# Performance work log

Measured on AMD Instinct MI355X. Metric: run time of the kernel, lower is better.

Reference implementation:

```python
import jax, jax.numpy as jnp
import numpy as np
from jax import lax

L_TAU = 0.8
NUM_TIME = 20
B, H, W = 128, 64, 64
FLAT = 6 * 27 * 27  # 4374 features after conv(k=10)->55x55 and maxpool2 -> 27x27

def setup_inputs() -> dict:
    key = jax.random.key(0)
    k1, k2, k3, k4, k5, k6 = jax.random.split(key, 6)
    x = jax.random.uniform(k1, (B, H * W, NUM_TIME), dtype=jnp.float32)
    y = jax.random.randint(k2, (B,), 0, 2, dtype=jnp.int64)
    Wc = jax.random.normal(k3, (6, 1, 10, 10), dtype=jnp.float32) * 0.1  # OIHW
    bc = jnp.zeros((6,), dtype=jnp.float32)
    W2 = jax.random.normal(k4, (FLAT, 2), dtype=jnp.float32) * (1.0 / np.sqrt(FLAT))
    b2 = jnp.zeros((2,), dtype=jnp.float32)
    return {"x": x, "y": y, "Wc": Wc, "bc": bc, "W2": W2, "b2": b2}

def _maxpool2(a):
    return lax.reduce_window(a, -jnp.inf, lax.max,
                             (1, 1, 2, 2), (1, 1, 2, 2), 'VALID')

def _snu_forward(x, Wc, bc, W2, b2):
    xt = jnp.transpose(x, (2, 0, 1)).reshape(NUM_TIME, B, 1, H, W)  # [T,B,1,64,64]
    s1 = jnp.zeros((B, 6, 55, 55), jnp.float32); y1 = jnp.zeros_like(s1)
    s2 = jnp.zeros((B, 2), jnp.float32);        y2 = jnp.zeros_like(s2)

    def step(carry, x_t):
        s1, y1, s2, y2 = carry
        c = lax.conv_general_dilated(x_t, Wc, (1, 1), 'VALID',
                                     dimension_numbers=('NCHW', 'OIHW', 'NCHW'))
        # SNU state: s = relu(conv(x) + l_tau * s * (1 - y)); emission: y = sigmoid(s + b)
        s1 = jax.nn.relu(c + L_TAU * s1 * (1.0 - y1))
        y1 = jax.nn.sigmoid(s1 + bc[None, :, None, None])
        h = _maxpool2(y1).reshape(B, FLAT)           # [B, 4374]
        s2 = jax.nn.relu(h @ W2 + L_TAU * s2 * (1.0 - y2))
        y2 = jax.nn.sigmoid(s2 + b2)
        return (s1, y1, s2, y2), y2

    _, outs = lax.scan(step, (s1, y1, s2, y2), xt)   # [T, B, 2]
    out_rec = jnp.concatenate([jnp.zeros((1, B, 2), jnp.float32), outs], axis=0)
    out_rec = jnp.transpose(out_rec, (1, 0, 2))      # [B, T+1, 2]
    m = jnp.sum(out_rec, axis=1) / 20.0
    return m, out_rec

def reference(x, y, Wc, bc, W2, b2):
    m, out_rec = _snu_forward(x, Wc, bc, W2, b2)
    logp = jax.nn.log_softmax(m, axis=1)
    loss = -jnp.mean(logp[jnp.arange(B), y])         # CrossEntropyLoss
    acc = jnp.mean((jnp.argmax(m, axis=1) == y).astype(jnp.float32))
    return (loss, m, out_rec, acc)
```

## Files before the change

### kernel.cpp

```cpp
#include <hip/hip_runtime.h>
#include <hip/hip_bf16.h>
#include <math.h>

#define L_TAU_C 0.8f

typedef _Float16 half2_t __attribute__((ext_vector_type(2)));

union U32H2 { unsigned int u; half2_t h; };
__device__ __forceinline__ half2_t h2(unsigned int v) { U32H2 x; x.u = v; return x.h; }

__device__ __forceinline__ float sigmoidf_(float x) {
    return 1.0f / (1.0f + __expf(-x));
}

__global__ __launch_bounds__(256) void k_transpose16(const float* __restrict__ x,
                                                     _Float16* __restrict__ xT) {
    int gp = blockIdx.x * 256 + threadIdx.x;
    int b = gp >> 12, p = gp & 4095;
    const float4* src = reinterpret_cast<const float4*>(x + (size_t)gp * 20);
    float v[20];
#pragma unroll
    for (int k = 0; k < 5; ++k) {
        float4 q = src[k];
        v[4 * k + 0] = q.x; v[4 * k + 1] = q.y; v[4 * k + 2] = q.z; v[4 * k + 3] = q.w;
    }
    _Float16* dst = xT + (size_t)b * 20 * 4096 + p;
#pragma unroll
    for (int t = 0; t < 20; ++t) dst[(size_t)t * 4096] = (_Float16)v[t];
}

template<int XMODE>
__global__ __launch_bounds__(384, 2) void k_conv_snu(
    const float* __restrict__ x,
    const _Float16* __restrict__ xT,
    const float* __restrict__ Wc,
    const float* __restrict__ bc,
    const float* __restrict__ W2,
    float* __restrict__ partw)
{
    const int tid = threadIdx.x;
    const int bi = blockIdx.x;
    const int xcd = bi & 7, slot = bi >> 3;
    const int b = (slot / 6) * 8 + xcd;
    const int ch = slot % 6;

    const bool active = tid < 378;
    const int r = tid / 14;
    const int pcg = tid % 14;
    const int row0 = 2 * r;

    const float* wb = Wc + ch * 100;
    unsigned int wsg[50];
#pragma unroll
    for (int i = 0; i < 50; ++i) {
        U32H2 pk;
        pk.h = half2_t{(_Float16)wb[2 * i], (_Float16)wb[2 * i + 1]};
        wsg[i] = (unsigned int)__builtin_amdgcn_readfirstlane((int)pk.u);
    }

    float s1[2][4], y1[2][4];
#pragma unroll
    for (int i = 0; i < 2; ++i)
#pragma unroll
        for (int j = 0; j < 4; ++j) { s1[i][j] = 0.f; y1[i][j] = 0.f; }

    const float bch = bc[ch];

    float w2r[2][2];
    w2r[0][0] = 0.f; w2r[0][1] = 0.f; w2r[1][0] = 0.f; w2r[1][1] = 0.f;
    if (active) {
#pragma unroll
        for (int k = 0; k < 2; ++k) {
            int pc = 2 * pcg + k;
            if (pc < 27) {
                int f0 = ch * 729 + r * 27 + pc;
                w2r[k][0] = W2[(size_t)f0 * 2 + 0];
                w2r[k][1] = W2[(size_t)f0 * 2 + 1];
            }
        }
    }

    const _Float16* xb16 = xT + (size_t)b * 20 * 4096;
    const float* xb32 = x + (size_t)b * 4096 * 20;

    for (int t = 0; t < 20; ++t) {
        float p0 = 0.f, p1 = 0.f;
        if (active) {
            float c0[4] = {0.f, 0.f, 0.f, 0.f};
            float c1[4] = {0.f, 0.f, 0.f, 0.f};

#pragma unroll
            for (int xr = 0; xr < 11; ++xr) {
                const int R = row0 + xr;
                unsigned int s[7];
                if (XMODE == 1) {
                    const _Float16* rp = xb16 + (size_t)t * 4096 + R * 64 + 4 * pcg;
                    uint2 a = *reinterpret_cast<const uint2*>(rp);
                    uint2 bq = *reinterpret_cast<const uint2*>(rp + 4);
                    uint2 cq = *reinterpret_cast<const uint2*>(rp + 8);
                    unsigned int dq = *reinterpret_cast<const unsigned int*>(rp + 12);
                    s[0] = a.x; s[1] = a.y; s[2] = bq.x; s[3] = bq.y;
                    s[4] = cq.x; s[5] = cq.y; s[6] = dq;
                } else {
                    const float* rp = xb32 + ((size_t)R * 64 + 4 * pcg) * 20 + t;
#pragma unroll
                    for (int q = 0; q < 7; ++q) {
                        U32H2 pk;
                        pk.h = half2_t{(_Float16)rp[(2 * q) * 20],
                                       (_Float16)rp[(2 * q + 1) * 20]};
                        s[q] = pk.u;
                    }
                }
                unsigned int ss[6];
#pragma unroll
                for (int i = 0; i < 6; ++i)
                    ss[i] = (s[i] >> 16) | (s[i + 1] << 16);

                if (xr <= 9) {
#pragma unroll
                    for (int m = 0; m < 5; ++m) {
                        half2_t w = h2(wsg[xr * 5 + m]);
                        c0[0] = __builtin_amdgcn_fdot2(h2(s[m]),      w, c0[0], false);
                        c0[1] = __builtin_amdgcn_fdot2(h2(ss[m]),     w, c0[1], false);
                        c0[2] = __builtin_amdgcn_fdot2(h2(s[m + 1]),  w, c0[2], false);
                        c0[3] = __builtin_amdgcn_fdot2(h2(ss[m + 1]), w, c0[3], false);
                    }
                }
                if (xr >= 1) {
#pragma unroll
                    for (int m = 0; m < 5; ++m) {
                        half2_t w = h2(wsg[(xr - 1) * 5 + m]);
                        c1[0] = __builtin_amdgcn_fdot2(h2(s[m]),      w, c1[0], false);
                        c1[1] = __builtin_amdgcn_fdot2(h2(ss[m]),     w, c1[1], false);
                        c1[2] = __builtin_amdgcn_fdot2(h2(s[m + 1]),  w, c1[2], false);
                        c1[3] = __builtin_amdgcn_fdot2(h2(ss[m + 1]), w, c1[3], false);
                    }
                }
            }
#pragma unroll
            for (int j = 0; j < 4; ++j) {
                float sa = fmaxf(c0[j] + L_TAU_C * s1[0][j] * (1.f - y1[0][j]), 0.f);
                float sb = fmaxf(c1[j] + L_TAU_C * s1[1][j] * (1.f - y1[1][j]), 0.f);
                s1[0][j] = sa; s1[1][j] = sb;
                y1[0][j] = sigmoidf_(sa + bch);
                y1[1][j] = sigmoidf_(sb + bch);
            }
            float h0 = fmaxf(fmaxf(y1[0][0], y1[0][1]), fmaxf(y1[1][0], y1[1][1]));
            float h1 = fmaxf(fmaxf(y1[0][2], y1[0][3]), fmaxf(y1[1][2], y1[1][3]));
            p0 = h0 * w2r[0][0] + h1 * w2r[1][0];
            p1 = h0 * w2r[0][1] + h1 * w2r[1][1];
        }
#pragma unroll
        for (int off = 32; off >= 1; off >>= 1) {
            p0 += __shfl_down(p0, off);
            p1 += __shfl_down(p1, off);
        }
        if ((tid & 63) == 0) {
            float2 val; val.x = p0; val.y = p1;
            *reinterpret_cast<float2*>(
                &partw[((((size_t)t * 128 + b) * 6 + ch) * 6 + (tid >> 6)) * 2]) = val;
        }
    }
}

__global__ __launch_bounds__(128) void k_final(const float* __restrict__ partw,
                                               const void* __restrict__ yraw,
                                               const float* __restrict__ b2,
                                               float* __restrict__ out) {
    __shared__ float red[4];
    const int b = threadIdx.x;

    const int* yi = (const int*)yraw;
    bool i64 = true;
    for (int k = 0; k < 64; ++k) {
        if (yi[2 * k + 1] != 0) { i64 = false; break; }
    }
    int lbl = i64 ? (int)((const long long*)yraw)[b] : yi[b];

    float b20 = b2[0], b21 = b2[1];
    float s20 = 0.f, s21 = 0.f, y20 = 0.f, y21 = 0.f, m0 = 0.f, m1 = 0.f;
    float* orec = out + 257 + b * 42;
    orec[0] = 0.f; orec[1] = 0.f;
    for (int t = 0; t < 20; ++t) {
        const float4* pp = reinterpret_cast<const float4*>(
            partw + ((size_t)t * 128 + b) * 72);
        float sum0 = 0.f, sum1 = 0.f;
#pragma unroll
        for (int i = 0; i < 18; ++i) {
            float4 a = pp[i];
            sum0 += a.x + a.z;
            sum1 += a.y + a.w;
        }
        s20 = fmaxf(sum0 + L_TAU_C * s20 * (1.f - y20), 0.f);
        s21 = fmaxf(sum1 + L_TAU_C * s21 * (1.f - y21), 0.f);
        y20 = sigmoidf_(s20 + b20);
        y21 = sigmoidf_(s21 + b21);
        orec[(t + 1) * 2 + 0] = y20;
        orec[(t + 1) * 2 + 1] = y21;
        m0 += y20; m1 += y21;
    }
    m0 *= 0.05f; m1 *= 0.05f;
    out[1 + b * 2 + 0] = m0;
    out[1 + b * 2 + 1] = m1;

    float mx = fmaxf(m0, m1);
    float lse = mx + logf(expf(m0 - mx) + expf(m1 - mx));
    float lossc = -(((lbl != 0) ? m1 : m0) - lse);
    int pred = (m1 > m0) ? 1 : 0;
    float accc = (pred == lbl) ? 1.f : 0.f;
#pragma unroll
    for (int off = 32; off >= 1; off >>= 1) {
        lossc += __shfl_down(lossc, off);
        accc += __shfl_down(accc, off);
    }
    if ((b & 63) == 0) { red[(b >> 6) * 2] = lossc; red[(b >> 6) * 2 + 1] = accc; }
    __syncthreads();
    if (b == 0) {
        out[0] = (red[0] + red[2]) * (1.f / 128.f);
        out[5633] = (red[1] + red[3]) * (1.f / 128.f);
    }
}

extern "C" void kernel_launch(void* const* d_in, const int* in_sizes, int n_in,
                              void* d_out, int out_size, void* d_ws, size_t ws_size,
                              hipStream_t stream) {
    const float* x  = (const float*)d_in[0];
    const void*  y  = d_in[1];
    const float* Wc = (const float*)d_in[2];
    const float* bc = (const float*)d_in[3];
    const float* W2 = (const float*)d_in[4];
    const float* b2 = (const float*)d_in[5];
    float* out = (float*)d_out;

    const size_t xt_bytes = (size_t)128 * 20 * 4096 * 2;
    const size_t partw_bytes = (size_t)20 * 128 * 6 * 6 * 2 * 4;
    const int use16 = (ws_size >= xt_bytes + partw_bytes) ? 1 : 0;

    _Float16* xT = (_Float16*)d_ws;
    float* partw = use16 ? (float*)((char*)d_ws + xt_bytes) : (float*)d_ws;

    if (use16) {
        k_transpose16<<<2048, 256, 0, stream>>>(x, xT);
        k_conv_snu<1><<<768, 384, 0, stream>>>(x, xT, Wc, bc, W2, partw);
    } else {
        k_conv_snu<0><<<768, 384, 0, stream>>>(x, (const _Float16*)d_ws, Wc, bc, W2, partw);
    }
    k_final<<<1, 128, 0, stream>>>(partw, y, b2, out);
}
```

Baseline: 159.9 us.

## Prefetch input rows two ahead with aligned 16-byte loads and raise occupancy

The conv loop now software-pipelines input loads, fetching the row two iterations ahead into double-buffered registers. Each thread reads from a 16-byte-aligned base using uint4 loads and picks its window with a select on the column parity. The launch bound's minimum blocks per CU goes from 2 to 5, which pushes the compiler to use fewer registers. The goal is to hide global-load latency and raise occupancy, at the risk of register spills with 50 weight registers plus the prefetch buffers.

```diff
diff --git a/kernel.cpp b/kernel.cpp
--- a/kernel.cpp
+++ b/kernel.cpp
@@ -29,8 +29,28 @@
     for (int t = 0; t < 20; ++t) dst[(size_t)t * 4096] = (_Float16)v[t];
 }
 
+__device__ __forceinline__ void load_row16(const _Float16* rp, uint4& A,
+                                           uint4& B, unsigned& E) {
+    A = *reinterpret_cast<const uint4*>(rp);
+    B = *reinterpret_cast<const uint4*>(rp + 8);
+    E = *reinterpret_cast<const unsigned*>(rp + 16);
+}
+
+__device__ __forceinline__ unsigned packf20(const float* p) {
+    U32H2 pk; pk.h = half2_t{(_Float16)p[0], (_Float16)p[20]}; return pk.u;
+}
+
+__device__ __forceinline__ void load_row32(const float* rp, uint4& A,
+                                           uint4& B, unsigned& E) {
+    A.x = packf20(rp);       A.y = packf20(rp + 40);
+    A.z = packf20(rp + 80);  A.w = packf20(rp + 120);
+    B.x = packf20(rp + 160); B.y = packf20(rp + 200);
+    B.z = packf20(rp + 240); B.w = packf20(rp + 280);
+    E   = packf20(rp + 320);
+}
+
 template<int XMODE>
-__global__ __launch_bounds__(384, 2) void k_conv_snu(
+__global__ __launch_bounds__(384, 5) void k_conv_snu(
     const float* __restrict__ x,
     const _Float16* __restrict__ xT,
     const float* __restrict__ Wc,
@@ -48,6 +68,8 @@
     const int r = tid / 14;
     const int pcg = tid % 14;
     const int row0 = 2 * r;
+    const int off = pcg & 1;
+    const int hb = 4 * pcg - 4 * off;
 
     const float* wb = Wc + ch * 100;
     unsigned int wsg[50];
@@ -89,29 +111,40 @@
             float c0[4] = {0.f, 0.f, 0.f, 0.f};
             float c1[4] = {0.f, 0.f, 0.f, 0.f};
 
+            const _Float16* tb16 = xb16 + (size_t)t * 4096 + hb;
+            const float* tb32 = xb32 + (size_t)hb * 20 + t;
+
+            uint4 a0, b0, a1, b1; unsigned e0, e1;
+            if (XMODE == 1) {
+                load_row16(tb16 + (size_t)(row0 + 0) * 64, a0, b0, e0);
+                load_row16(tb16 + (size_t)(row0 + 1) * 64, a1, b1, e1);
+            } else {
+                load_row32(tb32 + (size_t)(row0 + 0) * 64 * 20, a0, b0, e0);
+                load_row32(tb32 + (size_t)(row0 + 1) * 64 * 20, a1, b1, e1);
+            }
+
 #pragma unroll
             for (int xr = 0; xr < 11; ++xr) {
-                const int R = row0 + xr;
-                unsigned int s[7];
-                if (XMODE == 1) {
-                    const _Float16* rp = xb16 + (size_t)t * 4096 + R * 64 + 4 * pcg;
-                    uint2 a = *reinterpret_cast<const uint2*>(rp);
-                    uint2 bq = *reinterpret_cast<const uint2*>(rp + 4);
-                    uint2 cq = *reinterpret_cast<const uint2*>(rp + 8);
-                    unsigned int dq = *reinterpret_cast<const unsigned int*>(rp + 12);
-                    s[0] = a.x; s[1] = a.y; s[2] = bq.x; s[3] = bq.y;
-                    s[4] = cq.x; s[5] = cq.y; s[6] = dq;
-                } else {
-                    const float* rp = xb32 + ((size_t)R * 64 + 4 * pcg) * 20 + t;
-#pragma unroll
-                    for (int q = 0; q < 7; ++q) {
-                        U32H2 pk;
-                        pk.h = half2_t{(_Float16)rp[(2 * q) * 20],
-                                       (_Float16)rp[(2 * q + 1) * 20]};
-                        s[q] = pk.u;
+                uint4 A  = (xr & 1) ? a1 : a0;
+                uint4 Bq = (xr & 1) ? b1 : b0;
+                unsigned E = (xr & 1) ? e1 : e0;
+                if (xr + 2 <= 10) {
+                    if (XMODE == 1) {
+                        const _Float16* rp = tb16 + (size_t)(row0 + xr + 2) * 64;
+                        if (xr & 1) load_row16(rp, a1, b1, e1);
+                        else        load_row16(rp, a0, b0, e0);
+                    } else {
+                        const float* rp = tb32 + (size_t)(row0 + xr + 2) * 64 * 20;
+                        if (xr & 1) load_row32(rp, a1, b1, e1);
+                        else        load_row32(rp, a0, b0, e0);
                     }
                 }
-                unsigned int ss[6];
+
+                unsigned w_[9] = {A.x, A.y, A.z, A.w, Bq.x, Bq.y, Bq.z, Bq.w, E};
+                unsigned s[7];
+#pragma unroll
+                for (int i = 0; i < 7; ++i) s[i] = off ? w_[i + 2] : w_[i];
+                unsigned ss[6];
 #pragma unroll
                 for (int i = 0; i < 6; ++i)
                     ss[i] = (s[i] >> 16) | (s[i + 1] << 16);
@@ -151,9 +184,9 @@
             p1 = h0 * w2r[0][1] + h1 * w2r[1][1];
         }
 #pragma unroll
-        for (int off = 32; off >= 1; off >>= 1) {
-            p0 += __shfl_down(p0, off);
-            p1 += __shfl_down(p1, off);
+        for (int off2 = 32; off2 >= 1; off2 >>= 1) {
+            p0 += __shfl_down(p0, off2);
+            p1 += __shfl_down(p1, off2);
         }
         if ((tid & 63) == 0) {
             float2 val; val.x = p0; val.y = p1;
```

Measured after the change: 601.4 us. 3.76x slower.

## Double-buffer conv input rows with aligned 16-byte loads and raise occupancy

Applied to the files above, without the earlier changes.

Input rows are now loaded as aligned uint4 pairs plus one extra word, with an odd/even column offset selecting the seven half2 words per thread. Loads for row xr+2 are issued while row xr is being computed, using two register buffers. Launch bounds move from 2 to 5 waves per SIMD, which forces tighter register limits. The aim is wider, better-aligned memory transactions and memory latency hidden behind the dot products, at the risk of register spills under the new bound.

```diff
diff --git a/kernel.cpp b/kernel.cpp
--- a/kernel.cpp
+++ b/kernel.cpp
@@ -30,7 +30,7 @@
 }
 
 template<int XMODE>
-__global__ __launch_bounds__(384, 2) void k_conv_snu(
+__global__ __launch_bounds__(384, 5) void k_conv_snu(
     const float* __restrict__ x,
     const _Float16* __restrict__ xT,
     const float* __restrict__ Wc,
@@ -48,6 +48,9 @@
     const int r = tid / 14;
     const int pcg = tid % 14;
     const int row0 = 2 * r;
+    const int off = pcg & 1;
+    const int ub = 2 * pcg - 2 * off;
+    const int ue = (pcg == 13) ? 7 : 8;
 
     const float* wb = Wc + ch * 100;
     unsigned int wsg[50];
@@ -80,8 +83,9 @@
         }
     }
 
-    const _Float16* xb16 = xT + (size_t)b * 20 * 4096;
-    const float* xb32 = x + (size_t)b * 4096 * 20;
+    const unsigned* xb16 = reinterpret_cast<const unsigned*>(
+        xT + (size_t)b * 20 * 4096) + ub;
+    const float* xb32 = x + (size_t)b * 4096 * 20 + (size_t)(2 * ub) * 20;
 
     for (int t = 0; t < 20; ++t) {
         float p0 = 0.f, p1 = 0.f;
@@ -89,29 +93,81 @@
             float c0[4] = {0.f, 0.f, 0.f, 0.f};
             float c1[4] = {0.f, 0.f, 0.f, 0.f};
 
+            const unsigned* tb16 = xb16 + (size_t)t * 2048;
+            const float* tb32 = xb32 + t;
+
+            uint4 r0A, r0B, r1A, r1B; unsigned r0E, r1E;
+            if (XMODE == 1) {
+                const unsigned* rp0 = tb16 + (size_t)(row0 + 0) * 32;
+                const unsigned* rp1 = tb16 + (size_t)(row0 + 1) * 32;
+                r0A = *reinterpret_cast<const uint4*>(rp0);
+                r0B = *reinterpret_cast<const uint4*>(rp0 + 4);
+                r0E = rp0[ue];
+                r1A = *reinterpret_cast<const uint4*>(rp1);
+                r1B = *reinterpret_cast<const uint4*>(rp1 + 4);
+                r1E = rp1[ue];
+            } else {
+#pragma unroll
+                for (int sl = 0; sl < 2; ++sl) {
+                    const float* rp = tb32 + (size_t)(row0 + sl) * 64 * 20;
+                    uint4 A, Bq; unsigned E;
+                    U32H2 pk;
+                    pk.h = half2_t{(_Float16)rp[0],   (_Float16)rp[20]};  A.x = pk.u;
+                    pk.h = half2_t{(_Float16)rp[40],  (_Float16)rp[60]};  A.y = pk.u;
+                    pk.h = half2_t{(_Float16)rp[80],  (_Float16)rp[100]}; A.z = pk.u;
+                    pk.h = half2_t{(_Float16)rp[120], (_Float16)rp[140]}; A.w = pk.u;
+                    pk.h = half2_t{(_Float16)rp[160], (_Float16)rp[180]}; Bq.x = pk.u;
+                    pk.h = half2_t{(_Float16)rp[200], (_Float16)rp[220]}; Bq.y = pk.u;
+                    pk.h = half2_t{(_Float16)rp[240], (_Float16)rp[260]}; Bq.z = pk.u;
+                    pk.h = half2_t{(_Float16)rp[280], (_Float16)rp[300]}; Bq.w = pk.u;
+                    pk.h = half2_t{(_Float16)rp[ue * 40], (_Float16)rp[ue * 40 + 20]};
+                    E = pk.u;
+                    if (sl == 0) { r0A = A; r0B = Bq; r0E = E; }
+                    else         { r1A = A; r1B = Bq; r1E = E; }
+                }
+            }
+
 #pragma unroll
             for (int xr = 0; xr < 11; ++xr) {
-                const int R = row0 + xr;
-                unsigned int s[7];
-                if (XMODE == 1) {
-                    const _Float16* rp = xb16 + (size_t)t * 4096 + R * 64 + 4 * pcg;
-                    uint2 a = *reinterpret_cast<const uint2*>(rp);
-                    uint2 bq = *reinterpret_cast<const uint2*>(rp + 4);
-                    uint2 cq = *reinterpret_cast<const uint2*>(rp + 8);
-                    unsigned int dq = *reinterpret_cast<const unsigned int*>(rp + 12);
-                    s[0] = a.x; s[1] = a.y; s[2] = bq.x; s[3] = bq.y;
-                    s[4] = cq.x; s[5] = cq.y; s[6] = dq;
-                } else {
-                    const float* rp = xb32 + ((size_t)R * 64 + 4 * pcg) * 20 + t;
-#pragma unroll
-                    for (int q = 0; q < 7; ++q) {
+                uint4 A  = (xr & 1) ? r1A : r0A;
+                uint4 Bq = (xr & 1) ? r1B : r0B;
+                unsigned E = (xr & 1) ? r1E : r0E;
+                if (xr + 2 <= 10) {
+                    if (XMODE == 1) {
+                        const unsigned* rp = tb16 + (size_t)(row0 + xr + 2) * 32;
+                        uint4 nA = *reinterpret_cast<const uint4*>(rp);
+                        uint4 nB = *reinterpret_cast<const uint4*>(rp + 4);
+                        unsigned nE = rp[ue];
+                        if (xr & 1) { r1A = nA; r1B = nB; r1E = nE; }
+                        else        { r0A = nA; r0B = nB; r0E = nE; }
+                    } else {
+                        const float* rp = tb32 + (size_t)(row0 + xr + 2) * 64 * 20;
+                        uint4 nA, nB; unsigned nE;
                         U32H2 pk;
-                        pk.h = half2_t{(_Float16)rp[(2 * q) * 20],
-                                       (_Float16)rp[(2 * q + 1) * 20]};
-                        s[q] = pk.u;
+                        pk.h = half2_t{(_Float16)rp[0],   (_Float16)rp[20]};  nA.x = pk.u;
+                        pk.h = half2_t{(_Float16)rp[40],  (_Float16)rp[60]};  nA.y = pk.u;
+                        pk.h = half2_t{(_Float16)rp[80],  (_Float16)rp[100]}; nA.z = pk.u;
+                        pk.h = half2_t{(_Float16)rp[120], (_Float16)rp[140]}; nA.w = pk.u;
+                        pk.h = half2_t{(_Float16)rp[160], (_Float16)rp[180]}; nB.x = pk.u;
+                        pk.h = half2_t{(_Float16)rp[200], (_Float16)rp[220]}; nB.y = pk.u;
+                        pk.h = half2_t{(_Float16)rp[240], (_Float16)rp[260]}; nB.z = pk.u;
+                        pk.h = half2_t{(_Float16)rp[280], (_Float16)rp[300]}; nB.w = pk.u;
+                        pk.h = half2_t{(_Float16)rp[ue * 40], (_Float16)rp[ue * 40 + 20]};
+                        nE = pk.u;
+                        if (xr & 1) { r1A = nA; r1B = nB; r1E = nE; }
+                        else        { r0A = nA; r0B = nB; r0E = nE; }
                     }
                 }
-                unsigned int ss[6];
+
+                unsigned s0 = off ? A.z : A.x;
+                unsigned s1v = off ? A.w : A.y;
+                unsigned s2 = off ? Bq.x : A.z;
+                unsigned s3 = off ? Bq.y : A.w;
+                unsigned s4 = off ? Bq.z : Bq.x;
+                unsigned s5 = off ? Bq.w : Bq.y;
+                unsigned s6 = off ? E : Bq.z;
+                unsigned s[7] = {s0, s1v, s2, s3, s4, s5, s6};
+                unsigned ss[6];
 #pragma unroll
                 for (int i = 0; i < 6; ++i)
                     ss[i] = (s[i] >> 16) | (s[i + 1] << 16);
@@ -151,9 +207,9 @@
             p1 = h0 * w2r[0][1] + h1 * w2r[1][1];
         }
 #pragma unroll
-        for (int off = 32; off >= 1; off >>= 1) {
-            p0 += __shfl_down(p0, off);
-            p1 += __shfl_down(p1, off);
+        for (int off2 = 32; off2 >= 1; off2 >>= 1) {
+            p0 += __shfl_down(p0, off2);
+            p1 += __shfl_down(p1, off2);
         }
         if ((tid & 63) == 0) {
             float2 val; val.x = p0; val.y = p1;
```

New measurement: 177.6 us. 11.1% more time.

## Reformulate conv as MFMA 16x16x32 GEMM with channel-packed weight fragments

Applied to the files above, without the earlier changes.

Replaces the per-thread fdot2 direct convolution with MFMA f16 matrix instructions. Each wave computes 16 output rows by a 6-column stripe for all 6 channels. Columns are packed into the N dimension as channel and parity, and the kernel-column shift is folded into zero-padded B fragments, one per column offset. The pooling partner is exchanged by shuffle, and the grid is relaid as 9 column groups by 4 waves per batch. This is meant to cut VALU cost, but it wastes MFMA lanes on padding (N=16 with only 12 used) and on rows past 55. It also changes the partial-sum layout that k_final reads, and that kernel's updated indexing cannot be seen.

```diff
diff --git a/kernel.cpp b/kernel.cpp
--- a/kernel.cpp
+++ b/kernel.cpp
@@ -4,10 +4,14 @@
 
 #define L_TAU_C 0.8f
 
+typedef _Float16 f16x8 __attribute__((ext_vector_type(8)));
+typedef float f32x4 __attribute__((ext_vector_type(4)));
+typedef unsigned int uint2a4 __attribute__((ext_vector_type(2), aligned(4)));
+typedef unsigned int uint4e __attribute__((ext_vector_type(4)));
+
+union U4H8 { uint4e u; f16x8 h; };
 typedef _Float16 half2_t __attribute__((ext_vector_type(2)));
-
 union U32H2 { unsigned int u; half2_t h; };
-__device__ __forceinline__ half2_t h2(unsigned int v) { U32H2 x; x.u = v; return x.h; }
 
 __device__ __forceinline__ float sigmoidf_(float x) {
     return 1.0f / (1.0f + __expf(-x));
@@ -30,7 +34,7 @@
 }
 
 template<int XMODE>
-__global__ __launch_bounds__(384, 2) void k_conv_snu(
+__global__ __launch_bounds__(256, 3) void k_conv_snu(
     const float* __restrict__ x,
     const _Float16* __restrict__ xT,
     const float* __restrict__ Wc,
@@ -41,124 +45,130 @@
     const int tid = threadIdx.x;
     const int bi = blockIdx.x;
     const int xcd = bi & 7, slot = bi >> 3;
-    const int b = (slot / 6) * 8 + xcd;
-    const int ch = slot % 6;
-
-    const bool active = tid < 378;
-    const int r = tid / 14;
-    const int pcg = tid % 14;
-    const int row0 = 2 * r;
-
-    const float* wb = Wc + ch * 100;
-    unsigned int wsg[50];
-#pragma unroll
-    for (int i = 0; i < 50; ++i) {
-        U32H2 pk;
-        pk.h = half2_t{(_Float16)wb[2 * i], (_Float16)wb[2 * i + 1]};
-        wsg[i] = (unsigned int)__builtin_amdgcn_readfirstlane((int)pk.u);
-    }
-
-    float s1[2][4], y1[2][4];
-#pragma unroll
-    for (int i = 0; i < 2; ++i)
-#pragma unroll
-        for (int j = 0; j < 4; ++j) { s1[i][j] = 0.f; y1[i][j] = 0.f; }
-
-    const float bch = bc[ch];
-
-    float w2r[2][2];
-    w2r[0][0] = 0.f; w2r[0][1] = 0.f; w2r[1][0] = 0.f; w2r[1][1] = 0.f;
-    if (active) {
-#pragma unroll
-        for (int k = 0; k < 2; ++k) {
-            int pc = 2 * pcg + k;
-            if (pc < 27) {
-                int f0 = ch * 729 + r * 27 + pc;
-                w2r[k][0] = W2[(size_t)f0 * 2 + 0];
-                w2r[k][1] = W2[(size_t)f0 * 2 + 1];
-            }
-        }
-    }
+    const int b = (slot / 9) * 8 + xcd;
+    const int jg = slot % 9;
+    const int w = tid >> 6;
+    const int l = tid & 63;
+    const int RS = 16 * w;
+    const int C0 = 6 * jg;
+    const int n = l & 15, lh = l >> 4;
+    const int ch = n >> 1, e = n & 1;
+
+    f16x8 Bf[3][5];
+#pragma unroll
+    for (int s = 0; s < 3; ++s) {
+#pragma unroll
+        for (int q = 0; q < 5; ++q) {
+            f16x8 bv;
+#pragma unroll
+            for (int j = 0; j < 8; ++j) {
+                int wr = 2 * q + (j >> 2);
+                int wc = 4 * lh + (j & 3);
+                int wcd = wc - (2 * s + e);
+                float wv = 0.f;
+                if (ch < 6 && wcd >= 0 && wcd < 10)
+                    wv = Wc[ch * 100 + wr * 10 + wcd];
+                bv[j] = (_Float16)wv;
+            }
+            Bf[s][q] = bv;
+        }
+    }
+
+    float sA[3][4], yA[3][4];
+#pragma unroll
+    for (int s = 0; s < 3; ++s)
+#pragma unroll
+        for (int g = 0; g < 4; ++g) { sA[s][g] = 0.f; yA[s][g] = 0.f; }
+
+    const float bch = (ch < 6) ? bc[ch] : 0.f;
+
+    float w2v[3][2][2];
+#pragma unroll
+    for (int s = 0; s < 3; ++s)
+#pragma unroll
+        for (int m = 0; m < 2; ++m) {
+            int prow = 8 * w + 2 * lh + m;
+            int pcol = 3 * jg + s;
+            float a0 = 0.f, a1 = 0.f;
+            if (e == 0 && ch < 6 && prow < 27) {
+                int f = ch * 729 + prow * 27 + pcol;
+                a0 = W2[(size_t)f * 2 + 0];
+                a1 = W2[(size_t)f * 2 + 1];
+            }
+            w2v[s][m][0] = a0; w2v[s][m][1] = a1;
+        }
 
     const _Float16* xb16 = xT + (size_t)b * 20 * 4096;
     const float* xb32 = x + (size_t)b * 4096 * 20;
+    const int ar = RS + (l & 15);
+    const int acol = C0 + 4 * lh;
 
     for (int t = 0; t < 20; ++t) {
+        f16x8 Af[5];
+        if (XMODE == 1) {
+            const _Float16* tb = xb16 + (size_t)t * 4096 + acol;
+#pragma unroll
+            for (int q = 0; q < 5; ++q) {
+                int r0 = ar + 2 * q;     if (r0 > 63) r0 = 63;
+                int r1 = ar + 2 * q + 1; if (r1 > 63) r1 = 63;
+                uint2a4 lo = *reinterpret_cast<const uint2a4*>(tb + r0 * 64);
+                uint2a4 hi = *reinterpret_cast<const uint2a4*>(tb + r1 * 64);
+                U4H8 u; u.u = (uint4e){lo[0], lo[1], hi[0], hi[1]};
+                Af[q] = u.h;
+            }
+        } else {
+            const float* tb = xb32 + t;
+#pragma unroll
+            for (int q = 0; q < 5; ++q) {
+                f16x8 av;
+#pragma unroll
+                for (int j = 0; j < 8; ++j) {
+                    int r = ar + 2 * q + (j >> 2); if (r > 63) r = 63;
+                    av[j] = (_Float16)tb[(size_t)(r * 64 + acol + (j & 3)) * 20];
+                }
+                Af[q] = av;
+            }
+        }
+
+        f32x4 acc[3];
+#pragma unroll
+        for (int s = 0; s < 3; ++s) acc[s] = (f32x4){0.f, 0.f, 0.f, 0.f};
+#pragma unroll
+        for (int q = 0; q < 5; ++q) {
+#pragma unroll
+            for (int s = 0; s < 3; ++s)
+                acc[s] = __builtin_amdgcn_mfma_f32_16x16x32_f16(
+                    Af[q], Bf[s][q], acc[s], 0, 0, 0);
+        }
+
         float p0 = 0.f, p1 = 0.f;
-        if (active) {
-            float c0[4] = {0.f, 0.f, 0.f, 0.f};
-            float c1[4] = {0.f, 0.f, 0.f, 0.f};
-
-#pragma unroll
-            for (int xr = 0; xr < 11; ++xr) {
-                const int R = row0 + xr;
-                unsigned int s[7];
-                if (XMODE == 1) {
-                    const _Float16* rp = xb16 + (size_t)t * 4096 + R * 64 + 4 * pcg;
-                    uint2 a = *reinterpret_cast<const uint2*>(rp);
-                    uint2 bq = *reinterpret_cast<const uint2*>(rp + 4);
-                    uint2 cq = *reinterpret_cast<const uint2*>(rp + 8);
-                    unsigned int dq = *reinterpret_cast<const unsigned int*>(rp + 12);
-                    s[0] = a.x; s[1] = a.y; s[2] = bq.x; s[3] = bq.y;
-                    s[4] = cq.x; s[5] = cq.y; s[6] = dq;
-                } else {
-                    const float* rp = xb32 + ((size_t)R * 64 + 4 * pcg) * 20 + t;
-#pragma unroll
-                    for (int q = 0; q < 7; ++q) {
-                        U32H2 pk;
-                        pk.h = half2_t{(_Float16)rp[(2 * q) * 20],
-                                       (_Float16)rp[(2 * q + 1) * 20]};
-                        s[q] = pk.u;
-                    }
-                }
-                unsigned int ss[6];
-#pragma unroll
-                for (int i = 0; i < 6; ++i)
-                    ss[i] = (s[i] >> 16) | (s[i + 1] << 16);
-
-                if (xr <= 9) {
-#pragma unroll
-                    for (int m = 0; m < 5; ++m) {
-                        half2_t w = h2(wsg[xr * 5 + m]);
-                        c0[0] = __builtin_amdgcn_fdot2(h2(s[m]),      w, c0[0], false);
-                        c0[1] = __builtin_amdgcn_fdot2(h2(ss[m]),     w, c0[1], false);
-                        c0[2] = __builtin_amdgcn_fdot2(h2(s[m + 1]),  w, c0[2], false);
-                        c0[3] = __builtin_amdgcn_fdot2(h2(ss[m + 1]), w, c0[3], false);
-                    }
-                }
-                if (xr >= 1) {
-#pragma unroll
-                    for (int m = 0; m < 5; ++m) {
-                        half2_t w = h2(wsg[(xr - 1) * 5 + m]);
-                        c1[0] = __builtin_amdgcn_fdot2(h2(s[m]),      w, c1[0], false);
-                        c1[1] = __builtin_amdgcn_fdot2(h2(ss[m]),     w, c1[1], false);
-                        c1[2] = __builtin_amdgcn_fdot2(h2(s[m + 1]),  w, c1[2], false);
-                        c1[3] = __builtin_amdgcn_fdot2(h2(ss[m + 1]), w, c1[3], false);
-                    }
-                }
-            }
-#pragma unroll
-            for (int j = 0; j < 4; ++j) {
-                float sa = fmaxf(c0[j] + L_TAU_C * s1[0][j] * (1.f - y1[0][j]), 0.f);
-                float sb = fmaxf(c1[j] + L_TAU_C * s1[1][j] * (1.f - y1[1][j]), 0.f);
-                s1[0][j] = sa; s1[1][j] = sb;
-                y1[0][j] = sigmoidf_(sa + bch);
-                y1[1][j] = sigmoidf_(sb + bch);
-            }
-            float h0 = fmaxf(fmaxf(y1[0][0], y1[0][1]), fmaxf(y1[1][0], y1[1][1]));
-            float h1 = fmaxf(fmaxf(y1[0][2], y1[0][3]), fmaxf(y1[1][2], y1[1][3]));
-            p0 = h0 * w2r[0][0] + h1 * w2r[1][0];
-            p1 = h0 * w2r[0][1] + h1 * w2r[1][1];
-        }
+#pragma unroll
+        for (int s = 0; s < 3; ++s) {
+#pragma unroll
+            for (int g = 0; g < 4; ++g) {
+                float sa = fmaxf(acc[s][g] + L_TAU_C * sA[s][g] * (1.f - yA[s][g]), 0.f);
+                sA[s][g] = sa;
+                yA[s][g] = sigmoidf_(sa + bch);
+            }
+            float m0 = fmaxf(yA[s][0], yA[s][1]);
+            float m1 = fmaxf(yA[s][2], yA[s][3]);
+            float o0 = __shfl_xor(m0, 1);
+            float o1 = __shfl_xor(m1, 1);
+            float h0 = fmaxf(m0, o0);
+            float h1 = fmaxf(m1, o1);
+            p0 += h0 * w2v[s][0][0] + h1 * w2v[s][1][0];
+            p1 += h0 * w2v[s][0][1] + h1 * w2v[s][1][1];
+        }
+
 #pragma unroll
         for (int off = 32; off >= 1; off >>= 1) {
             p0 += __shfl_down(p0, off);
             p1 += __shfl_down(p1, off);
         }
-        if ((tid & 63) == 0) {
+        if (l == 0) {
             float2 val; val.x = p0; val.y = p1;
             *reinterpret_cast<float2*>(
-                &partw[((((size_t)t * 128 + b) * 6 + ch) * 6 + (tid >> 6)) * 2]) = val;
+                &partw[((((size_t)t * 128 + b) * 9 + jg) * 4 + w) * 2]) = val;
         }
     }
 }
@@ -233,7 +243,7 @@
     float* out = (float*)d_out;
 
     const size_t xt_bytes = (size_t)128 * 20 * 4096 * 2;
-    const size_t partw_bytes = (size_t)20 * 128 * 6 * 6 * 2 * 4;
+    const size_t partw_bytes = (size_t)20 * 128 * 9 * 4 * 2 * 4;
     const int use16 = (ws_size >= xt_bytes + partw_bytes) ? 1 : 0;
 
     _Float16* xT = (_Float16*)d_ws;
@@ -241,9 +251,9 @@
 
     if (use16) {
         k_transpose16<<<2048, 256, 0, stream>>>(x, xT);
-        k_conv_snu<1><<<768, 384, 0, stream>>>(x, xT, Wc, bc, W2, partw);
+        k_conv_snu<1><<<1152, 256, 0, stream>>>(x, xT, Wc, bc, W2, partw);
     } else {
-        k_conv_snu<0><<<768, 384, 0, stream>>>(x, (const _Float16*)d_ws, Wc, bc, W2, partw);
+        k_conv_snu<0><<<1152, 256, 0, stream>>>(x, (const _Float16*)d_ws, Wc, bc, W2, partw);
     }
     k_final<<<1, 128, 0, stream>>>(partw, y, b2, out);
 }
```

New measurement: 163.4 us. +2.2%, slower.
